# Performance work log

Measured on AMD Instinct MI355X. Metric: run time of the kernel, lower is better.

The kernel has to match this reference:

```python
import jax, jax.numpy as jnp
import numpy as np


def setup_inputs() -> dict:
    key = jax.random.key(0)
    k1, k2, k3 = jax.random.split(key, 3)
    B, S, D = 2, 2048, 1024
    N_COMPRESS, RANK = 64, 64
    x = jax.random.normal(k1, (B, S, D), dtype=jnp.float32)
    router_w = jax.random.normal(k2, (N_COMPRESS, D), dtype=jnp.float32) * (1.0 / np.sqrt(D))
    # compress neurons (orthogonal-init in torch; gaussian scaled is fine for a numeric baseline)
    neurons = jax.random.normal(k3, (N_COMPRESS, D, RANK), dtype=jnp.float32) * (1.0 / np.sqrt(D))
    return {"x": x, "router_w": router_w, "neurons": neurons}


TOP_K = 2


def reference(x, router_w, neurons):
    # x: [B,S,D], router_w: [N,D], neurons: [N,D,R]
    B, S, D = x.shape
    R = neurons.shape[-1]
    scores = jnp.einsum('bsd,nd->bsn', x, router_w)            # [B,S,N]
    topk_scores, topk_idx = jax.lax.top_k(scores, TOP_K)       # [B,S,K]
    topk_weights = jax.nn.softmax(topk_scores, axis=-1)        # [B,S,K]
    output = jnp.zeros((B, S, R), dtype=x.dtype)
    for i in range(TOP_K):  # small fixed loop, mirrors original slot-wise combine
        idx = topk_idx[:, :, i]                                # [B,S]
        sel = neurons[idx]                                     # [B,S,D,R] gather
        proj = jnp.einsum('bsd,bsdr->bsr', x, sel)             # per-token matvec
        output = output + topk_weights[:, :, i:i + 1] * proj
    return output, topk_idx, topk_weights
```

## Files before the change

kernel.cpp:

```cpp
#include <hip/hip_runtime.h>
#include <hip/hip_bf16.h>


typedef unsigned short u16;
typedef unsigned int u32;
typedef __attribute__((ext_vector_type(8))) short short8;
typedef __attribute__((ext_vector_type(4))) float f32x4;

__device__ __forceinline__ float bf2f(u16 u) {
    u32 v = ((u32)u) << 16; float f; __builtin_memcpy(&f, &v, 4); return f;
}
__device__ __forceinline__ u16 f2bf(float f) {
    u32 u; __builtin_memcpy(&u, &f, 4);
    u32 r = u + 0x7fff + ((u >> 16) & 1);
    return (u16)(r >> 16);
}
__device__ __forceinline__ u32 pack2(float a, float b) {
    return ((u32)f2bf(b) << 16) | (u32)f2bf(a);
}

#define T_TOKENS 4096
#define DDIM 1024
#define NEXP 64
#define RDIM 64
#define LCAP 1024
#define OUT_IDX_OFF 262144
#define OUT_W_OFF 270336

struct LdBF {
    const u16* p;
    __device__ __forceinline__ float4 ld4(size_t i) const {
        ushort4 v = *(const ushort4*)(p + i);
        return make_float4(bf2f(v.x), bf2f(v.y), bf2f(v.z), bf2f(v.w));
    }
    __device__ __forceinline__ float ld1(size_t i) const { return bf2f(p[i]); }
};
struct LdF32 {
    const float* p;
    __device__ __forceinline__ float4 ld4(size_t i) const { return *(const float4*)(p + i); }
    __device__ __forceinline__ float ld1(size_t i) const { return p[i]; }
};

__device__ __forceinline__ int detect_f32(const u16* x, int* lds_cnt) {
    if (threadIdx.x == 0) *lds_cnt = 0;
    __syncthreads();
    if (threadIdx.x < 256) {
        unsigned e = (x[threadIdx.x] >> 7) & 0xFF;
        if (e >= 0x68 && e <= 0x88) atomicAdd(lds_cnt, 1);
    }
    __syncthreads();
    int f = (*lds_cnt < 200) ? 1 : 0;
    __syncthreads();
    return f;
}

template <class LD>
__device__ __forceinline__ void score_body(LD xld, LD rwld,
                                           float* xs , float* wt ,
                                           float* sc ,
                                           float* out, float* wsW,
                                           int* wsCnt, int* wsList) {
    const int tid = threadIdx.x;
    const size_t t0 = (size_t)blockIdx.x * 8;
    const int wv = tid >> 6;
    const int lane = tid & 63;
    const int tg = lane & 1;
    const int eg = (lane >> 1) & 7;
    const int kql = (lane >> 4) & 3;
    const int dd = 4 * kql + 16 * wv;
    const int kc0 = blockIdx.x & 15;

    const int sm = tid >> 4;
    const int sd4 = (tid & 15) * 4;

    float acc[4][8];
#pragma unroll
    for (int mi = 0; mi < 4; ++mi)
#pragma unroll
        for (int ei = 0; ei < 8; ++ei) acc[mi][ei] = 0.f;

    float4 px;
    if (tid < 128) px = xld.ld4((t0 + sm) * DDIM + kc0 * 64 + sd4);
    float4 pw[4];
#pragma unroll
    for (int h = 0; h < 4; ++h) {
        int i4 = tid + h * 256;
        pw[h] = rwld.ld4((size_t)(i4 >> 4) * DDIM + kc0 * 64 + (i4 & 15) * 4);
    }

    for (int i = 0; i < 16; ++i) {
        if (i > 0) __syncthreads();
        if (tid < 128) *(float4*)&xs[sm * 68 + sd4] = px;
#pragma unroll
        for (int h = 0; h < 4; ++h) {
            int i4 = tid + h * 256;
            *(float4*)&wt[(i4 >> 4) * 68 + (i4 & 15) * 4] = pw[h];
        }
        __syncthreads();

        if (i < 15) {
            int kn = ((i + 1 + kc0) & 15) * 64;
            if (tid < 128) px = xld.ld4((t0 + sm) * DDIM + kn + sd4);
#pragma unroll
            for (int h = 0; h < 4; ++h) {
                int i4 = tid + h * 256;
                pw[h] = rwld.ld4((size_t)(i4 >> 4) * DDIM + kn + (i4 & 15) * 4);
            }
        }

        float4 xv[4], wv4[8];
#pragma unroll
        for (int mi = 0; mi < 4; ++mi)
            xv[mi] = *(const float4*)&xs[(tg + 2 * mi) * 68 + dd];
#pragma unroll
        for (int ei = 0; ei < 8; ++ei)
            wv4[ei] = *(const float4*)&wt[(eg + 8 * ei) * 68 + dd];
#pragma unroll
        for (int mi = 0; mi < 4; ++mi)
#pragma unroll
            for (int ei = 0; ei < 8; ++ei)
                acc[mi][ei] += xv[mi].x * wv4[ei].x + xv[mi].y * wv4[ei].y +
                               xv[mi].z * wv4[ei].z + xv[mi].w * wv4[ei].w;
    }

#pragma unroll
    for (int mi = 0; mi < 4; ++mi)
#pragma unroll
        for (int ei = 0; ei < 8; ++ei) {
            float v = acc[mi][ei];
            v += __shfl_xor(v, 16, 64);
            v += __shfl_xor(v, 32, 64);
            acc[mi][ei] = v;
        }
    __syncthreads();

    for (int w = 0; w < 4; ++w) {
        if (wv == w && kql == 0) {
#pragma unroll
            for (int mi = 0; mi < 4; ++mi)
#pragma unroll
                for (int ei = 0; ei < 8; ++ei) {
                    int idx = (tg + 2 * mi) * 65 + eg + 8 * ei;
                    sc[idx] = (w == 0) ? acc[mi][ei] : sc[idx] + acc[mi][ei];
                }
        }
        __syncthreads();
    }

    if (tid < 8) {
        const float* s = &sc[tid * 65];
        float best = -1e30f, secv = -1e30f;
        int bi = 0, si = 0;
        for (int j = 0; j < NEXP; ++j) {
            float v = s[j];
            if (v > best) { secv = best; si = bi; best = v; bi = j; }
            else if (v > secv) { secv = v; si = j; }
        }
        float w0 = 1.0f / (1.0f + expf(secv - best));
        float w1 = 1.0f - w0;
        size_t t = t0 + tid;
        out[OUT_IDX_OFF + t * 2 + 0] = (float)bi;
        out[OUT_IDX_OFF + t * 2 + 1] = (float)si;
        out[OUT_W_OFF + t * 2 + 0] = w0;
        out[OUT_W_OFF + t * 2 + 1] = w1;
        wsW[t * 2 + 0] = w0;
        wsW[t * 2 + 1] = w1;
        int p0 = atomicAdd(&wsCnt[bi], 1);
        if (p0 < LCAP) wsList[bi * LCAP + p0] = (int)(t * 2 + 0);
        int p1 = atomicAdd(&wsCnt[si], 1);
        if (p1 < LCAP) wsList[si * LCAP + p1] = (int)(t * 2 + 1);
    }
}

__global__ __launch_bounds__(256, 2) void score_topk(const void* x, const void* rw,
                                                     float* out, float* wsW,
                                                     int* wsCnt, int* wsList) {
    __shared__ float xs[8 * 68];
    __shared__ float wt[64 * 68];
    __shared__ float sc[8 * 65];
    __shared__ int dc;
    int f = detect_f32((const u16*)x, &dc);
    if (f)
        score_body(LdF32{(const float*)x}, LdF32{(const float*)rw}, xs, wt, sc, out, wsW, wsCnt, wsList);
    else
        score_body(LdBF{(const u16*)x}, LdBF{(const u16*)rw}, xs, wt, sc, out, wsW, wsCnt, wsList);
}

template <class LD>
__device__ __forceinline__ void egemm_body(LD xld, LD nld,
                                           const int* wsCnt, const int* wsList,
                                           float* P,
                                           u16* Ab , u16* Bb ,
                                           int* eL ) {
    const int tid = threadIdx.x;
    const int e = blockIdx.x >> 3;
    const int oct = blockIdx.x & 7;
    const int cntE = min(wsCnt[e], LCAP);
    if (cntE <= 0) return;
    const int wv = tid >> 6;
    const int lane = tid & 63;
    const int l15 = lane & 15, quad = lane >> 4;
    const size_t nbase = (size_t)e * (DDIM * RDIM);
    const int k0 = oct * 128;

    for (int j = tid; j < cntE; j += 256) eL[j] = wsList[e * LCAP + j];

    {
        const int rq = tid & 15;
        const int kpB = tid >> 4;
        u32* bb = (u32*)Bb;
#pragma unroll
        for (int h = 0; h < 4; ++h) {
            int kp = kpB + h * 16;
            float4 g0 = nld.ld4(nbase + (size_t)(k0 + 2 * kp) * RDIM + rq * 4);
            float4 g1 = nld.ld4(nbase + (size_t)(k0 + 2 * kp + 1) * RDIM + rq * 4);
            bb[(rq * 4 + 0) * 68 + kp] = pack2(g0.x, g1.x);
            bb[(rq * 4 + 1) * 68 + kp] = pack2(g0.y, g1.y);
            bb[(rq * 4 + 2) * 68 + kp] = pack2(g0.z, g1.z);
            bb[(rq * 4 + 3) * 68 + kp] = pack2(g0.w, g1.w);
        }
    }
    __syncthreads();

    const int rowA = tid >> 4;
    const int kqA = tid & 15;
    const int ntiles = (cntE + 15) >> 4;

    float4 a0, a1;
    {
        int t2r = eL[min(rowA, cntE - 1)];
        size_t xrow = (size_t)(t2r >> 1) * DDIM + k0;
        a0 = xld.ld4(xrow + kqA * 8);
        a1 = xld.ld4(xrow + kqA * 8 + 4);
    }

    for (int ti = 0; ti < ntiles; ++ti) {
        const int base = ti * 16;
        const int valid = min(16, cntE - base);
        if (ti > 0) __syncthreads();
        {
            uint4 w;
            w.x = pack2(a0.x, a0.y);
            w.y = pack2(a0.z, a0.w);
            w.z = pack2(a1.x, a1.y);
            w.w = pack2(a1.z, a1.w);
            *(uint4*)&((u32*)Ab)[rowA * 68 + kqA * 4] = w;
        }
        __syncthreads();
        if (ti + 1 < ntiles) {
            int t2r = eL[min(base + 16 + rowA, cntE - 1)];
            size_t xrow = (size_t)(t2r >> 1) * DDIM + k0;
            a0 = xld.ld4(xrow + kqA * 8);
            a1 = xld.ld4(xrow + kqA * 8 + 4);
        }

        f32x4 acc = {0.f, 0.f, 0.f, 0.f};
#pragma unroll
        for (int ko = 0; ko < 4; ++ko) {
            int kofs = ko * 32 + quad * 8;
            short8 bfr = *(const short8*)&Bb[(16 * wv + l15) * 136 + kofs];
            short8 af = *(const short8*)&Ab[l15 * 136 + kofs];
            acc = __builtin_amdgcn_mfma_f32_16x16x32_bf16(af, bfr, acc, 0, 0, 0);
        }

#pragma unroll
        for (int reg = 0; reg < 4; ++reg) {
            int m = quad * 4 + reg;
            if (m < valid) {
                int t2 = eL[base + m];
                P[(size_t)t2 * 512 + oct * 64 + 16 * wv + l15] = acc[reg];
            }
        }
    }
}

__global__ __launch_bounds__(256, 2) void expert_gemm(const void* x, const void* neurons,
                                                      const int* wsCnt, const int* wsList,
                                                      float* P) {
    __shared__ u16 Ab[16 * 136];
    __shared__ u16 Bb[64 * 136];
    __shared__ int eL[LCAP];
    __shared__ int dc;
    int f = detect_f32((const u16*)x, &dc);
    if (f)
        egemm_body(LdF32{(const float*)x}, LdF32{(const float*)neurons}, wsCnt, wsList, P, Ab, Bb, eL);
    else
        egemm_body(LdBF{(const u16*)x}, LdBF{(const u16*)neurons}, wsCnt, wsList, P, Ab, Bb, eL);
}

__global__ __launch_bounds__(256) void combine(const float* P, const float* wsW,
                                               float* out) {
    int i = blockIdx.x * 256 + threadIdx.x;
    int t = i >> 6, r = i & 63;
    const float* p0 = P + (size_t)(2 * t) * 512 + r;
    const float* p1 = P + (size_t)(2 * t + 1) * 512 + r;
    float s0 = 0.f, s1 = 0.f;
#pragma unroll
    for (int o = 0; o < 8; ++o) {
        s0 += p0[o * 64];
        s1 += p1[o * 64];
    }
    out[i] = wsW[2 * t] * s0 + wsW[2 * t + 1] * s1;
}

extern "C" void kernel_launch(void* const* d_in, const int* in_sizes, int n_in,
                              void* d_out, int out_size, void* d_ws, size_t ws_size,
                              hipStream_t stream) {
    const void* x = d_in[0];
    const void* rw = d_in[1];
    const void* neurons = d_in[2];
    float* out = (float*)d_out;

    char* wsc = (char*)d_ws;
    float* wsW = (float*)wsc;
    int* wsCnt = (int*)(wsc + 32 * 1024);
    int* wsList = (int*)((char*)wsCnt + 256);
    float* P = (float*)(wsc + (1 << 20));

    hipMemsetAsync(wsCnt, 0, 256, stream);
    score_topk<<<512, 256, 0, stream>>>(x, rw, out, wsW, wsCnt, wsList);
    expert_gemm<<<512, 256, 0, stream>>>(x, neurons, wsCnt, wsList, P);
    combine<<<1024, 256, 0, stream>>>(P, wsW, out);
}
```

Before: 126.1 us.

## Double-buffer LDS and prefetch three chunks ahead in score kernel

```diff
diff --git a/kernel.cpp b/kernel.cpp
--- a/kernel.cpp
+++ b/kernel.cpp
@@ -53,6 +53,48 @@
     __syncthreads();
     return f;
 }
+
+#define SC_ISSUE(chunk, s)                                                       \
+    {                                                                            \
+        int kn_ = (((chunk) + kc0) & 15) * 64;                                   \
+        if (tid < 128) px[s] = xld.ld4((t0 + sm) * DDIM + kn_ + sd4);            \
+        _Pragma("unroll")                                                        \
+        for (int h = 0; h < 4; ++h) {                                            \
+            int i4 = tid + h * 256;                                              \
+            pw[s][h] = rwld.ld4((size_t)(i4 >> 4) * DDIM + kn_ + (i4 & 15) * 4); \
+        }                                                                        \
+    }
+
+#define SC_WRITEBUF(buf, s)                                                      \
+    {                                                                            \
+        float* xsb_ = xs + (buf) * (8 * 68);                                     \
+        float* wtb_ = wt + (buf) * (64 * 68);                                    \
+        if (tid < 128) *(float4*)&xsb_[sm * 68 + sd4] = px[s];                   \
+        _Pragma("unroll")                                                        \
+        for (int h = 0; h < 4; ++h) {                                            \
+            int i4 = tid + h * 256;                                              \
+            *(float4*)&wtb_[(i4 >> 4) * 68 + (i4 & 15) * 4] = pw[s][h];          \
+        }                                                                        \
+    }
+
+#define SC_COMPUTE(buf)                                                          \
+    {                                                                            \
+        const float* xsb_ = xs + (buf) * (8 * 68);                               \
+        const float* wtb_ = wt + (buf) * (64 * 68);                              \
+        float4 xv[4], wv4[8];                                                    \
+        _Pragma("unroll")                                                        \
+        for (int mi = 0; mi < 4; ++mi)                                           \
+            xv[mi] = *(const float4*)&xsb_[(tg + 2 * mi) * 68 + dd];             \
+        _Pragma("unroll")                                                        \
+        for (int ei = 0; ei < 8; ++ei)                                           \
+            wv4[ei] = *(const float4*)&wtb_[(eg + 8 * ei) * 68 + dd];            \
+        _Pragma("unroll")                                                        \
+        for (int mi = 0; mi < 4; ++mi)                                           \
+            _Pragma("unroll")                                                    \
+            for (int ei = 0; ei < 8; ++ei)                                       \
+                acc[mi][ei] += xv[mi].x * wv4[ei].x + xv[mi].y * wv4[ei].y +     \
+                               xv[mi].z * wv4[ei].z + xv[mi].w * wv4[ei].w;      \
+    }
 
 template <class LD>
 __device__ __forceinline__ void score_body(LD xld, LD rwld,
@@ -79,48 +121,21 @@
 #pragma unroll
         for (int ei = 0; ei < 8; ++ei) acc[mi][ei] = 0.f;
 
-    float4 px;
-    if (tid < 128) px = xld.ld4((t0 + sm) * DDIM + kc0 * 64 + sd4);
-    float4 pw[4];
-#pragma unroll
-    for (int h = 0; h < 4; ++h) {
-        int i4 = tid + h * 256;
-        pw[h] = rwld.ld4((size_t)(i4 >> 4) * DDIM + kc0 * 64 + (i4 & 15) * 4);
-    }
-
+    float4 px[3];
+    float4 pw[3][4];
+
+    SC_ISSUE(0, 0);
+    SC_ISSUE(1, 1);
+    SC_ISSUE(2, 2);
+    SC_WRITEBUF(0, 0);
+    __syncthreads();
+
+#pragma unroll
     for (int i = 0; i < 16; ++i) {
-        if (i > 0) __syncthreads();
-        if (tid < 128) *(float4*)&xs[sm * 68 + sd4] = px;
-#pragma unroll
-        for (int h = 0; h < 4; ++h) {
-            int i4 = tid + h * 256;
-            *(float4*)&wt[(i4 >> 4) * 68 + (i4 & 15) * 4] = pw[h];
-        }
+        if (i < 15) SC_WRITEBUF((i + 1) & 1, (i + 1) % 3);
+        if (i < 13) SC_ISSUE(i + 3, i % 3);
+        SC_COMPUTE(i & 1);
         __syncthreads();
-
-        if (i < 15) {
-            int kn = ((i + 1 + kc0) & 15) * 64;
-            if (tid < 128) px = xld.ld4((t0 + sm) * DDIM + kn + sd4);
-#pragma unroll
-            for (int h = 0; h < 4; ++h) {
-                int i4 = tid + h * 256;
-                pw[h] = rwld.ld4((size_t)(i4 >> 4) * DDIM + kn + (i4 & 15) * 4);
-            }
-        }
-
-        float4 xv[4], wv4[8];
-#pragma unroll
-        for (int mi = 0; mi < 4; ++mi)
-            xv[mi] = *(const float4*)&xs[(tg + 2 * mi) * 68 + dd];
-#pragma unroll
-        for (int ei = 0; ei < 8; ++ei)
-            wv4[ei] = *(const float4*)&wt[(eg + 8 * ei) * 68 + dd];
-#pragma unroll
-        for (int mi = 0; mi < 4; ++mi)
-#pragma unroll
-            for (int ei = 0; ei < 8; ++ei)
-                acc[mi][ei] += xv[mi].x * wv4[ei].x + xv[mi].y * wv4[ei].y +
-                               xv[mi].z * wv4[ei].z + xv[mi].w * wv4[ei].w;
     }
 
 #pragma unroll
@@ -132,7 +147,6 @@
             v += __shfl_xor(v, 32, 64);
             acc[mi][ei] = v;
         }
-    __syncthreads();
 
     for (int w = 0; w < 4; ++w) {
         if (wv == w && kql == 0) {
@@ -175,8 +189,8 @@
 __global__ __launch_bounds__(256, 2) void score_topk(const void* x, const void* rw,
                                                      float* out, float* wsW,
                                                      int* wsCnt, int* wsList) {
-    __shared__ float xs[8 * 68];
-    __shared__ float wt[64 * 68];
+    __shared__ float xs[2 * 8 * 68];
+    __shared__ float wt[2 * 64 * 68];
     __shared__ float sc[8 * 65];
     __shared__ int dc;
     int f = detect_f32((const u16*)x, &dc);
```

Measured after the change: 292.5 us. 2.32x slower.

## Split router score GEMM over K halves and move top-k into separate kernel

Applied to the files above, without the earlier changes.

```diff
diff --git a/kernel.cpp b/kernel.cpp
--- a/kernel.cpp
+++ b/kernel.cpp
@@ -57,18 +57,19 @@
 template <class LD>
 __device__ __forceinline__ void score_body(LD xld, LD rwld,
                                            float* xs , float* wt ,
-                                           float* sc ,
-                                           float* out, float* wsW,
-                                           int* wsCnt, int* wsList) {
+                                           float* sc , float* Sb) {
     const int tid = threadIdx.x;
-    const size_t t0 = (size_t)blockIdx.x * 8;
+    const int g = blockIdx.x >> 1;
+    const int kh = blockIdx.x & 1;
+    const size_t t0 = (size_t)g * 8;
+    const int kbase = kh * 512;
     const int wv = tid >> 6;
     const int lane = tid & 63;
     const int tg = lane & 1;
     const int eg = (lane >> 1) & 7;
     const int kql = (lane >> 4) & 3;
     const int dd = 4 * kql + 16 * wv;
-    const int kc0 = blockIdx.x & 15;
+    const int kc0 = blockIdx.x & 7;
 
     const int sm = tid >> 4;
     const int sd4 = (tid & 15) * 4;
@@ -80,15 +81,15 @@
         for (int ei = 0; ei < 8; ++ei) acc[mi][ei] = 0.f;
 
     float4 px;
-    if (tid < 128) px = xld.ld4((t0 + sm) * DDIM + kc0 * 64 + sd4);
+    if (tid < 128) px = xld.ld4((t0 + sm) * DDIM + kbase + kc0 * 64 + sd4);
     float4 pw[4];
 #pragma unroll
     for (int h = 0; h < 4; ++h) {
         int i4 = tid + h * 256;
-        pw[h] = rwld.ld4((size_t)(i4 >> 4) * DDIM + kc0 * 64 + (i4 & 15) * 4);
-    }
-
-    for (int i = 0; i < 16; ++i) {
+        pw[h] = rwld.ld4((size_t)(i4 >> 4) * DDIM + kbase + kc0 * 64 + (i4 & 15) * 4);
+    }
+
+    for (int i = 0; i < 8; ++i) {
         if (i > 0) __syncthreads();
         if (tid < 128) *(float4*)&xs[sm * 68 + sd4] = px;
 #pragma unroll
@@ -98,8 +99,8 @@
         }
         __syncthreads();
 
-        if (i < 15) {
-            int kn = ((i + 1 + kc0) & 15) * 64;
+        if (i < 7) {
+            int kn = kbase + ((i + 1 + kc0) & 7) * 64;
             if (tid < 128) px = xld.ld4((t0 + sm) * DDIM + kn + sd4);
 #pragma unroll
             for (int h = 0; h < 4; ++h) {
@@ -147,43 +148,60 @@
         __syncthreads();
     }
 
-    if (tid < 8) {
-        const float* s = &sc[tid * 65];
-        float best = -1e30f, secv = -1e30f;
-        int bi = 0, si = 0;
-        for (int j = 0; j < NEXP; ++j) {
-            float v = s[j];
-            if (v > best) { secv = best; si = bi; best = v; bi = j; }
-            else if (v > secv) { secv = v; si = j; }
-        }
-        float w0 = 1.0f / (1.0f + expf(secv - best));
-        float w1 = 1.0f - w0;
-        size_t t = t0 + tid;
-        out[OUT_IDX_OFF + t * 2 + 0] = (float)bi;
-        out[OUT_IDX_OFF + t * 2 + 1] = (float)si;
-        out[OUT_W_OFF + t * 2 + 0] = w0;
-        out[OUT_W_OFF + t * 2 + 1] = w1;
-        wsW[t * 2 + 0] = w0;
-        wsW[t * 2 + 1] = w1;
-        int p0 = atomicAdd(&wsCnt[bi], 1);
-        if (p0 < LCAP) wsList[bi * LCAP + p0] = (int)(t * 2 + 0);
-        int p1 = atomicAdd(&wsCnt[si], 1);
-        if (p1 < LCAP) wsList[si * LCAP + p1] = (int)(t * 2 + 1);
-    }
-}
-
-__global__ __launch_bounds__(256, 2) void score_topk(const void* x, const void* rw,
-                                                     float* out, float* wsW,
-                                                     int* wsCnt, int* wsList) {
+    if (tid < 128) {
+        int t = tid >> 4, e4 = (tid & 15) * 4;
+        const float* s = &sc[t * 65 + e4];
+        float4 v = make_float4(s[0], s[1], s[2], s[3]);
+        *(float4*)&Sb[((size_t)kh * T_TOKENS + t0 + t) * 64 + e4] = v;
+    }
+}
+
+__global__ __launch_bounds__(256, 4) void score_part(const void* x, const void* rw,
+                                                     float* Sb) {
     __shared__ float xs[8 * 68];
     __shared__ float wt[64 * 68];
     __shared__ float sc[8 * 65];
     __shared__ int dc;
     int f = detect_f32((const u16*)x, &dc);
     if (f)
-        score_body(LdF32{(const float*)x}, LdF32{(const float*)rw}, xs, wt, sc, out, wsW, wsCnt, wsList);
+        score_body(LdF32{(const float*)x}, LdF32{(const float*)rw}, xs, wt, sc, Sb);
     else
-        score_body(LdBF{(const u16*)x}, LdBF{(const u16*)rw}, xs, wt, sc, out, wsW, wsCnt, wsList);
+        score_body(LdBF{(const u16*)x}, LdBF{(const u16*)rw}, xs, wt, sc, Sb);
+}
+
+__global__ __launch_bounds__(256) void topk_softmax(const float* Sb, float* out,
+                                                    float* wsW, int* wsCnt,
+                                                    int* wsList) {
+    int t = blockIdx.x * 256 + threadIdx.x;
+    const float* s0 = Sb + (size_t)t * 64;
+    const float* s1 = Sb + ((size_t)T_TOKENS + t) * 64;
+    float best = -1e30f, secv = -1e30f;
+    int bi = 0, si = 0;
+    for (int j = 0; j < NEXP; j += 4) {
+        float4 a = *(const float4*)(s0 + j);
+        float4 b = *(const float4*)(s1 + j);
+        float v0 = a.x + b.x, v1 = a.y + b.y, v2 = a.z + b.z, v3 = a.w + b.w;
+        if (v0 > best) { secv = best; si = bi; best = v0; bi = j; }
+        else if (v0 > secv) { secv = v0; si = j; }
+        if (v1 > best) { secv = best; si = bi; best = v1; bi = j + 1; }
+        else if (v1 > secv) { secv = v1; si = j + 1; }
+        if (v2 > best) { secv = best; si = bi; best = v2; bi = j + 2; }
+        else if (v2 > secv) { secv = v2; si = j + 2; }
+        if (v3 > best) { secv = best; si = bi; best = v3; bi = j + 3; }
+        else if (v3 > secv) { secv = v3; si = j + 3; }
+    }
+    float w0 = 1.0f / (1.0f + expf(secv - best));
+    float w1 = 1.0f - w0;
+    out[OUT_IDX_OFF + (size_t)t * 2 + 0] = (float)bi;
+    out[OUT_IDX_OFF + (size_t)t * 2 + 1] = (float)si;
+    out[OUT_W_OFF + (size_t)t * 2 + 0] = w0;
+    out[OUT_W_OFF + (size_t)t * 2 + 1] = w1;
+    wsW[t * 2 + 0] = w0;
+    wsW[t * 2 + 1] = w1;
+    int p0 = atomicAdd(&wsCnt[bi], 1);
+    if (p0 < LCAP) wsList[bi * LCAP + p0] = t * 2 + 0;
+    int p1 = atomicAdd(&wsCnt[si], 1);
+    if (p1 < LCAP) wsList[si * LCAP + p1] = t * 2 + 1;
 }
 
 template <class LD>
@@ -315,10 +333,12 @@
     float* wsW = (float*)wsc;
     int* wsCnt = (int*)(wsc + 32 * 1024);
     int* wsList = (int*)((char*)wsCnt + 256);
-    float* P = (float*)(wsc + (1 << 20));
+    float* Sb = (float*)(wsc + (1 << 20));
+    float* P = (float*)(wsc + (4 << 20));
 
     hipMemsetAsync(wsCnt, 0, 256, stream);
-    score_topk<<<512, 256, 0, stream>>>(x, rw, out, wsW, wsCnt, wsList);
+    score_part<<<1024, 256, 0, stream>>>(x, rw, Sb);
+    topk_softmax<<<16, 256, 0, stream>>>(Sb, out, wsW, wsCnt, wsList);
     expert_gemm<<<512, 256, 0, stream>>>(x, neurons, wsCnt, wsList, P);
     combine<<<1024, 256, 0, stream>>>(P, wsW, out);
 }
```

Measured after the change: 125.4 us. Within noise of the previous version (-0.6%).
